# Kernel optimization log

Measured on AMD Instinct MI355X. Metric: run time of the kernel, lower is better.

## Reference

```python
import jax, jax.numpy as jnp
import numpy as np

TEMPERATURE = 0.1
NEG_INF = -1e30


def setup_inputs() -> dict:
    key = jax.random.key(0)
    kf, kl = jax.random.split(key)
    N, D = 8192, 128
    features = jax.random.normal(kf, (N, D), dtype=jnp.float32)
    # labels in [-1, 80): -1 marks background rows that are filtered out
    labels = jax.random.randint(kl, (N,), -1, 80)
    return {"features": features, "labels": labels}


def reference(features, labels):
    N = labels.shape[0]
    fg = labels >= 0  # [N]

    # F.normalize(p=2, dim=1): x / max(||x||, eps)
    norm = jnp.maximum(jnp.linalg.norm(features, axis=1, keepdims=True), 1e-12)
    f = features / norm

    sim = jnp.matmul(f, f.T) / TEMPERATURE  # [N, N]

    pair_fg = fg[:, None] & fg[None, :]
    eye = jnp.eye(N, dtype=bool)
    label_eq = labels[:, None] == labels[None, :]
    pos_mask = pair_fg & label_eq & ~eye          # positives (same label, not self)
    all_mask = pair_fg & ~eye                     # pos | neg == everything but self (within fg)

    # row-wise masked max, clamped to [-20, 20] as in the original
    max_sim = jnp.max(jnp.where(all_mask, sim, NEG_INF), axis=1)
    max_sim = jnp.clip(max_sim, -20.0, 20.0)

    e = jnp.exp(sim - max_sim[:, None])           # cos-sim/temp is bounded, no overflow
    pos_sum = jnp.clip(jnp.sum(jnp.where(pos_mask, e, 0.0), axis=1), 1e-6, 1e6)
    all_sum = jnp.clip(jnp.sum(jnp.where(all_mask, e, 0.0), axis=1), 1e-6, 1e6)

    loss_i = jnp.minimum(-jnp.log(pos_sum / all_sum), 10.0)  # clamp(max=10)

    # rows contributing to the mean: fg rows with at least one positive
    valid = fg & (jnp.sum(pos_mask, axis=1) > 0)
    n_valid = jnp.sum(valid)
    mean_loss = jnp.sum(jnp.where(valid, loss_i, 0.0)) / jnp.maximum(n_valid, 1).astype(jnp.float32)

    ok = (jnp.sum(fg) >= 2) & (n_valid > 0)
    return jnp.where(ok, mean_loss, jnp.float32(0.0))
```

## Files before the change

### kernel.cpp

```cpp
#include <hip/hip_runtime.h>

#define N 8192
#define D 128
#define CHUNK 256
#define NCC (N / CHUNK)
#define TILE_IT (CHUNK / 128)
#define NBIN 81
#define PBLK 512

typedef unsigned short u16;
typedef __attribute__((ext_vector_type(8))) __bf16 bf16x8;
typedef __attribute__((ext_vector_type(4))) float f32x4;

#define PREP_SCALE 3.7982889979f

__device__ __forceinline__ u16 f2bf(float x) {
  unsigned u = __float_as_uint(x);
  u += 0x7fff + ((u >> 16) & 1);
  return (u16)(u >> 16);
}

__global__ __launch_bounds__(256) void cpe_prep(const float* __restrict__ feat,
                                                const int* __restrict__ labels,
                                                u16* __restrict__ fhi,
                                                int* __restrict__ slab,
                                                unsigned* __restrict__ ctrR,
                                                float* __restrict__ acc3,
                                                unsigned* __restrict__ ctr2) {
  __shared__ int hist[4][NBIN], part[4][NBIN], lbase[NBIN], lpos[16];
  const int tid = threadIdx.x;
  const int w = tid >> 6, l = tid & 63;
  const int bid = blockIdx.x;
  if (tid < NBIN) {
#pragma unroll
    for (int cp = 0; cp < 4; ++cp) { hist[cp][tid] = 0; part[cp][tid] = 0; }
  }
  if (bid == 0) {
    if (tid < NCC) ctrR[tid] = 0u;
    else if (tid < NCC + 4) acc3[tid - NCC] = 0.0f;
    else if (tid == NCC + 4) *ctr2 = 0u;
  }
  __syncthreads();
  const int myBase = bid * 16;
  for (int j = tid; j < N; j += 256) {
    const int lab = labels[j] + 1;
    atomicAdd(&hist[w][lab], 1);
    if (j < myBase) atomicAdd(&part[w][lab], 1);
  }
  __syncthreads();
  if (tid < NBIN) {
    hist[0][tid] += hist[1][tid] + hist[2][tid] + hist[3][tid];
    part[0][tid] += part[1][tid] + part[2][tid] + part[3][tid];
  }
  __syncthreads();
  if (tid == 0) {
    int s = 0;
    for (int b = 0; b < NBIN; ++b) { lbase[b] = s; s += hist[0][b]; }
  }
  __syncthreads();
  if (tid < 16) {
    const int L = labels[myBase + tid] + 1;
    int pos = lbase[L] + part[0][L];
    for (int k = 0; k < tid; ++k) pos += (labels[myBase + k] + 1 == L) ? 1 : 0;
    lpos[tid] = pos;
    slab[pos] = L - 1;
  }
  __syncthreads();
#pragma unroll
  for (int rr = 0; rr < 4; ++rr) {
    const int k = w * 4 + rr;
    const float2 x = *(const float2*)&feat[(myBase + k) * D + l * 2];
    float s = x.x * x.x + x.y * x.y;
#pragma unroll
    for (int sh = 1; sh < 64; sh <<= 1) s += __shfl_xor(s, sh);
    const float inv = PREP_SCALE / fmaxf(sqrtf(s), 1e-12f);
    const int pos = lpos[k];
    *(ushort2*)&fhi[pos * D + l * 2] = make_ushort2(f2bf(x.x * inv), f2bf(x.y * inv));
  }
}

__global__ __launch_bounds__(256, 2) void cpe_main(
    const u16* __restrict__ fhi, const int* __restrict__ slab,
    float2* __restrict__ partials, unsigned* __restrict__ ctrR,
    float* __restrict__ acc3, unsigned* __restrict__ ctr2,
    float* __restrict__ out) {
  __shared__ __align__(16) u16 Bh[128 * 128];
  __shared__ int Lab[CHUNK];
  __shared__ float red[3][4];
  __shared__ int isLast;
  const int rt = blockIdx.x, cc = blockIdx.y;
  const int tid = threadIdx.x;
  const int w = tid >> 6, l = tid & 63, q = l >> 4, m = l & 15;
  const int r0w = rt * 256 + w * 64;
  const int cbase0 = cc * CHUNK;

  Lab[tid] = slab[cbase0 + tid];

  const int labi_lo = slab[r0w], labi_hi = slab[r0w + 63];

  bf16x8 Ah[4][4];
  int labi[4][4];
#pragma unroll
  for (int tr = 0; tr < 4; ++tr) {
    const int row = r0w + tr * 16 + m;
#pragma unroll
    for (int ks = 0; ks < 4; ++ks)
      Ah[tr][ks] = *(const bf16x8*)&fhi[row * D + ks * 32 + q * 8];
#pragma unroll
    for (int v = 0; v < 4; ++v) labi[tr][v] = slab[r0w + tr * 16 + q * 4 + v];
  }

  float ps[4][4], as_[4][4];
#pragma unroll
  for (int tr = 0; tr < 4; ++tr)
#pragma unroll
    for (int v = 0; v < 4; ++v) { ps[tr][v] = 0.f; as_[tr][v] = 0.f; }

  for (int it = 0; it < TILE_IT; ++it) {
    const int cbase = cbase0 + it * 128;
    __syncthreads();
#pragma unroll
    for (int n = 0; n < 8; ++n) {
      const int r = w * 32 + n * 4 + q;
      const int c = m ^ (r & 15);
      const u16* gh = &fhi[(size_t)(cbase + r) * D + c * 8];
      __builtin_amdgcn_global_load_lds(
          (const __attribute__((address_space(1))) unsigned*)gh,
          (__attribute__((address_space(3))) unsigned*)&Bh[(w * 512 + n * 64) * 8],
          16, 0, 0);
    }
    __syncthreads();

    for (int ct = 0; ct < 8; ++ct) {
      const int tb = it * 128 + ct * 16;
      const int labj_lo = Lab[tb], labj_hi = Lab[tb + 15];
      if (labj_hi < 0) continue;
      const bool slow = (labj_lo < 0) | ((labj_hi >= labi_lo) & (labj_lo <= labi_hi));
      const int jj = ct * 16 + m;
      f32x4 acc[4];
#pragma unroll
      for (int tr = 0; tr < 4; ++tr) acc[tr] = (f32x4){0.f, 0.f, 0.f, 0.f};
#pragma unroll
      for (int ks = 0; ks < 4; ++ks) {
        const int off = jj * 128 + ((ks * 4 + q) ^ m) * 8;
        const bf16x8 bh = *(const bf16x8*)&Bh[off];
#pragma unroll
        for (int tr = 0; tr < 4; ++tr)
          acc[tr] = __builtin_amdgcn_mfma_f32_16x16x32_bf16(Ah[tr][ks], bh, acc[tr], 0, 0, 0);
      }
      if (!slow) {
#pragma unroll
        for (int tr = 0; tr < 4; ++tr)
#pragma unroll
          for (int v = 0; v < 4; ++v)
            as_[tr][v] += __builtin_amdgcn_exp2f(acc[tr][v]);
      } else {
        const int labj = Lab[tb + m];
        const bool fgj = labj >= 0;
        const int jbase = cbase + ct * 16;
#pragma unroll
        for (int tr = 0; tr < 4; ++tr) {
          if (jbase == r0w + tr * 16) {
#pragma unroll
            for (int v = 0; v < 4; ++v) {
              const float e = __builtin_amdgcn_exp2f(acc[tr][v]);
              const float em = (fgj && (m != q * 4 + v)) ? e : 0.0f;
              as_[tr][v] += em;
              ps[tr][v] += (labj == labi[tr][v]) ? em : 0.0f;
            }
          } else {
#pragma unroll
            for (int v = 0; v < 4; ++v) {
              const float e = __builtin_amdgcn_exp2f(acc[tr][v]);
              const float em = fgj ? e : 0.0f;
              as_[tr][v] += em;
              ps[tr][v] += (labj == labi[tr][v]) ? em : 0.0f;
            }
          }
        }
      }
    }
  }

#pragma unroll
  for (int tr = 0; tr < 4; ++tr)
#pragma unroll
    for (int v = 0; v < 4; ++v) {
      float vp = ps[tr][v], va = as_[tr][v];
#pragma unroll
      for (int s = 1; s < 16; s <<= 1) {
        vp += __shfl_xor(vp, s);
        va += __shfl_xor(va, s);
      }
      if (m == 0)
        partials[(size_t)cc * N + r0w + tr * 16 + q * 4 + v] = make_float2(vp, va);
    }

  __syncthreads();
  if (tid == 0) {
    __threadfence();
    isLast = (atomicAdd(&ctrR[rt], 1u) == NCC - 1) ? 1 : 0;
  }
  __syncthreads();
  if (isLast) {
    __threadfence();
    const int r = rt * 256 + tid;
    float psr = 0.f, asr = 0.f;
#pragma unroll 4
    for (int c = 0; c < NCC; ++c) {
      union { unsigned long long u; float2 f; } cv;
      cv.u = __hip_atomic_load((const unsigned long long*)&partials[(size_t)c * N + r],
                               __ATOMIC_RELAXED, __HIP_MEMORY_SCOPE_AGENT);
      psr += cv.f.x;
      asr += cv.f.y;
    }
    const bool fg = slab[r] >= 0;
    const bool valid = fg && (psr > 0.f);
    const float loss = fminf(logf(asr / psr), 10.0f);
    float v0 = valid ? loss : 0.f;
    float v1 = valid ? 1.f : 0.f;
    float v2 = fg ? 1.f : 0.f;
#pragma unroll
    for (int s = 1; s < 64; s <<= 1) {
      v0 += __shfl_xor(v0, s);
      v1 += __shfl_xor(v1, s);
      v2 += __shfl_xor(v2, s);
    }
    if (l == 0) { red[0][w] = v0; red[1][w] = v1; red[2][w] = v2; }
    __syncthreads();
    if (tid == 0) {
      atomicAdd(&acc3[0], red[0][0] + red[0][1] + red[0][2] + red[0][3]);
      atomicAdd(&acc3[1], red[1][0] + red[1][1] + red[1][2] + red[1][3]);
      atomicAdd(&acc3[2], red[2][0] + red[2][1] + red[2][2] + red[2][3]);
      __threadfence();
      if (atomicAdd(ctr2, 1u) == 31u) {
        const float ls = atomicAdd(&acc3[0], 0.0f);
        const float nv = atomicAdd(&acc3[1], 0.0f);
        const float nf = atomicAdd(&acc3[2], 0.0f);
        out[0] = (nf >= 2.0f && nv > 0.0f) ? ls / fmaxf(nv, 1.0f) : 0.0f;
      }
    }
  }
}

extern "C" void kernel_launch(void* const* d_in, const int* in_sizes, int n_in,
                              void* d_out, int out_size, void* d_ws, size_t ws_size,
                              hipStream_t stream) {
  const float* feat = (const float*)d_in[0];
  const int* labels = (const int*)d_in[1];
  float* out = (float*)d_out;
  char* ws = (char*)d_ws;
  u16* fhi = (u16*)ws;
  float2* partials = (float2*)(ws + (size_t)N * D * 2);
  char* tail = ws + (size_t)N * D * 2 + (size_t)NCC * N * 8;
  int* slab = (int*)tail;
  unsigned* ctrR = (unsigned*)(tail + N * 4);
  float* acc3 = (float*)(tail + N * 4 + 128);
  unsigned* ctr2 = (unsigned*)(tail + N * 4 + 256);

  cpe_prep<<<PBLK, 256, 0, stream>>>(feat, labels, fhi, slab, ctrR, acc3, ctr2);
  cpe_main<<<dim3(N / 256, NCC), 256, 0, stream>>>(fhi, slab, partials, ctrR,
                                                   acc3, ctr2, out);
}
```

Baseline: 124.1 us.

## Double column chunk and move row reduction into a separate kernel

Column chunk width goes from 256 to 512, which halves the number of column blocks and partial sums. The per-row last-block detection (atomic counters, threadfences and the serialized tail inside the main kernel) is removed. A third kernel now reduces the partials per row and does the final mean. This trades an extra launch for a simpler main kernel with fewer blocks and no cross-block signalling.

```diff
diff --git a/kernel.cpp b/kernel.cpp
--- a/kernel.cpp
+++ b/kernel.cpp
@@ -2,7 +2,7 @@
 
 #define N 8192
 #define D 128
-#define CHUNK 256
+#define CHUNK 512
 #define NCC (N / CHUNK)
 #define TILE_IT (CHUNK / 128)
 #define NBIN 81
@@ -24,9 +24,7 @@
                                                 const int* __restrict__ labels,
                                                 u16* __restrict__ fhi,
                                                 int* __restrict__ slab,
-                                                unsigned* __restrict__ ctrR,
-                                                float* __restrict__ acc3,
-                                                unsigned* __restrict__ ctr2) {
+                                                float* __restrict__ acc3) {
   __shared__ int hist[4][NBIN], part[4][NBIN], lbase[NBIN], lpos[16];
   const int tid = threadIdx.x;
   const int w = tid >> 6, l = tid & 63;
@@ -35,11 +33,7 @@
 #pragma unroll
     for (int cp = 0; cp < 4; ++cp) { hist[cp][tid] = 0; part[cp][tid] = 0; }
   }
-  if (bid == 0) {
-    if (tid < NCC) ctrR[tid] = 0u;
-    else if (tid < NCC + 4) acc3[tid - NCC] = 0.0f;
-    else if (tid == NCC + 4) *ctr2 = 0u;
-  }
+  if (bid == 0 && tid < 4) acc3[tid] = 0.0f;
   __syncthreads();
   const int myBase = bid * 16;
   for (int j = tid; j < N; j += 256) {
@@ -81,13 +75,9 @@
 
 __global__ __launch_bounds__(256, 2) void cpe_main(
     const u16* __restrict__ fhi, const int* __restrict__ slab,
-    float2* __restrict__ partials, unsigned* __restrict__ ctrR,
-    float* __restrict__ acc3, unsigned* __restrict__ ctr2,
-    float* __restrict__ out) {
+    float2* __restrict__ partials) {
   __shared__ __align__(16) u16 Bh[128 * 128];
   __shared__ int Lab[CHUNK];
-  __shared__ float red[3][4];
-  __shared__ int isLast;
   const int rt = blockIdx.x, cc = blockIdx.y;
   const int tid = threadIdx.x;
   const int w = tid >> 6, l = tid & 63, q = l >> 4, m = l & 15;
@@ -95,6 +85,7 @@
   const int cbase0 = cc * CHUNK;
 
   Lab[tid] = slab[cbase0 + tid];
+  Lab[tid + 256] = slab[cbase0 + 256 + tid];
 
   const int labi_lo = slab[r0w], labi_hi = slab[r0w + 63];
 
@@ -195,50 +186,47 @@
       if (m == 0)
         partials[(size_t)cc * N + r0w + tr * 16 + q * 4 + v] = make_float2(vp, va);
     }
-
-  __syncthreads();
-  if (tid == 0) {
+}
+
+__global__ __launch_bounds__(256) void cpe_rows(const float2* __restrict__ partials,
+                                                const int* __restrict__ slab,
+                                                float* __restrict__ acc3,
+                                                float* __restrict__ out) {
+  const int r = blockIdx.x * 256 + threadIdx.x;
+  float psr = 0.f, asr = 0.f;
+#pragma unroll
+  for (int c = 0; c < NCC; ++c) {
+    const float2 p = partials[(size_t)c * N + r];
+    psr += p.x;
+    asr += p.y;
+  }
+  const bool fg = slab[r] >= 0;
+  const bool valid = fg && (psr > 0.f);
+  const float loss = fminf(logf(asr / psr), 10.0f);
+  float v0 = valid ? loss : 0.f;
+  float v1 = valid ? 1.f : 0.f;
+  float v2 = fg ? 1.f : 0.f;
+#pragma unroll
+  for (int s = 1; s < 64; s <<= 1) {
+    v0 += __shfl_xor(v0, s);
+    v1 += __shfl_xor(v1, s);
+    v2 += __shfl_xor(v2, s);
+  }
+  __shared__ float red[3][4];
+  const int w = threadIdx.x >> 6, l = threadIdx.x & 63;
+  if (l == 0) { red[0][w] = v0; red[1][w] = v1; red[2][w] = v2; }
+  __syncthreads();
+  if (threadIdx.x == 0) {
+    atomicAdd(&acc3[0], red[0][0] + red[0][1] + red[0][2] + red[0][3]);
+    atomicAdd(&acc3[1], red[1][0] + red[1][1] + red[1][2] + red[1][3]);
+    atomicAdd(&acc3[2], red[2][0] + red[2][1] + red[2][2] + red[2][3]);
     __threadfence();
-    isLast = (atomicAdd(&ctrR[rt], 1u) == NCC - 1) ? 1 : 0;
-  }
-  __syncthreads();
-  if (isLast) {
-    __threadfence();
-    const int r = rt * 256 + tid;
-    float psr = 0.f, asr = 0.f;
-#pragma unroll 4
-    for (int c = 0; c < NCC; ++c) {
-      union { unsigned long long u; float2 f; } cv;
-      cv.u = __hip_atomic_load((const unsigned long long*)&partials[(size_t)c * N + r],
-                               __ATOMIC_RELAXED, __HIP_MEMORY_SCOPE_AGENT);
-      psr += cv.f.x;
-      asr += cv.f.y;
-    }
-    const bool fg = slab[r] >= 0;
-    const bool valid = fg && (psr > 0.f);
-    const float loss = fminf(logf(asr / psr), 10.0f);
-    float v0 = valid ? loss : 0.f;
-    float v1 = valid ? 1.f : 0.f;
-    float v2 = fg ? 1.f : 0.f;
-#pragma unroll
-    for (int s = 1; s < 64; s <<= 1) {
-      v0 += __shfl_xor(v0, s);
-      v1 += __shfl_xor(v1, s);
-      v2 += __shfl_xor(v2, s);
-    }
-    if (l == 0) { red[0][w] = v0; red[1][w] = v1; red[2][w] = v2; }
-    __syncthreads();
-    if (tid == 0) {
-      atomicAdd(&acc3[0], red[0][0] + red[0][1] + red[0][2] + red[0][3]);
-      atomicAdd(&acc3[1], red[1][0] + red[1][1] + red[1][2] + red[1][3]);
-      atomicAdd(&acc3[2], red[2][0] + red[2][1] + red[2][2] + red[2][3]);
-      __threadfence();
-      if (atomicAdd(ctr2, 1u) == 31u) {
-        const float ls = atomicAdd(&acc3[0], 0.0f);
-        const float nv = atomicAdd(&acc3[1], 0.0f);
-        const float nf = atomicAdd(&acc3[2], 0.0f);
-        out[0] = (nf >= 2.0f && nv > 0.0f) ? ls / fmaxf(nv, 1.0f) : 0.0f;
-      }
+    const unsigned old = atomicAdd((unsigned*)&acc3[3], 1u);
+    if (old == gridDim.x - 1) {
+      const float ls = atomicAdd(&acc3[0], 0.0f);
+      const float nv = atomicAdd(&acc3[1], 0.0f);
+      const float nf = atomicAdd(&acc3[2], 0.0f);
+      out[0] = (nf >= 2.0f && nv > 0.0f) ? ls / fmaxf(nv, 1.0f) : 0.0f;
     }
   }
 }
@@ -254,11 +242,9 @@
   float2* partials = (float2*)(ws + (size_t)N * D * 2);
   char* tail = ws + (size_t)N * D * 2 + (size_t)NCC * N * 8;
   int* slab = (int*)tail;
-  unsigned* ctrR = (unsigned*)(tail + N * 4);
-  float* acc3 = (float*)(tail + N * 4 + 128);
-  unsigned* ctr2 = (unsigned*)(tail + N * 4 + 256);
-
-  cpe_prep<<<PBLK, 256, 0, stream>>>(feat, labels, fhi, slab, ctrR, acc3, ctr2);
-  cpe_main<<<dim3(N / 256, NCC), 256, 0, stream>>>(fhi, slab, partials, ctrR,
-                                                   acc3, ctr2, out);
-}
+  float* acc3 = (float*)(tail + N * 4);
+
+  cpe_prep<<<PBLK, 256, 0, stream>>>(feat, labels, fhi, slab, acc3);
+  cpe_main<<<dim3(N / 256, NCC), 256, 0, stream>>>(fhi, slab, partials);
+  cpe_rows<<<N / 256, 256, 0, stream>>>(partials, slab, acc3, out);
+}
```

Measured after the change: 103.6 us. 1.2x faster.
